# Kernel optimization log

Hardware: AMD Instinct MI355X
Metric: run time of the kernel (lower is better)

The kernel has to match this reference:

```python
import jax, jax.numpy as jnp
import numpy as np

B_, C_, NH_, WS_, HID_ = 8, 512, 16, 7, 2048
HH, WW = 56, 56


def _rel_pos_index(ws):
    coords = np.stack(np.meshgrid(np.arange(ws), np.arange(ws), indexing='ij'))  # (2,ws,ws)
    cf = coords.reshape(2, -1)
    rc = (cf[:, :, None] - cf[:, None, :]).transpose(1, 2, 0)  # (ws2,ws2,2)
    rc[..., 0] += ws - 1
    rc[..., 1] += ws - 1
    rc[..., 0] *= 2 * ws - 1
    return jnp.asarray(rc.sum(-1).reshape(-1))  # (ws2*ws2,)


def _ln(x, g, b, eps):
    mu = x.mean(-1, keepdims=True)
    var = ((x - mu) ** 2).mean(-1, keepdims=True)
    return (x - mu) * jax.lax.rsqrt(var + eps) * g + b


def setup_inputs() -> dict:
    key = jax.random.key(0)
    ks = jax.random.split(key, 8)
    s = lambda k, shape: (jax.random.normal(k, shape, jnp.float32) * 0.02)
    return {
        'x': jax.random.normal(ks[0], (B_, HH * WW, C_), jnp.float32),
        'H': HH, 'W': WW,
        'norm1_g': jnp.ones((C_,), jnp.float32), 'norm1_b': jnp.zeros((C_,), jnp.float32),
        'norm2_g': jnp.ones((C_,), jnp.float32), 'norm2_b': jnp.zeros((C_,), jnp.float32),
        'qkv_w': s(ks[1], (3 * C_, C_)), 'qkv_b': jnp.zeros((3 * C_,), jnp.float32),
        'rpb': s(ks[2], ((2 * WS_ - 1) ** 2, NH_)),
        'fc1_w': s(ks[3], (HID_, C_)), 'fc1_b': jnp.zeros((HID_,), jnp.float32),
        'dw_w': s(ks[4], (HID_, 1, 3, 3)), 'dw_b': jnp.zeros((HID_,), jnp.float32),
        'fc2_w': s(ks[5], (C_, HID_)), 'fc2_b': jnp.zeros((C_,), jnp.float32),
    }


def reference(x, H, W, norm1_g, norm1_b, norm2_g, norm2_b, qkv_w, qkv_b, rpb,
              fc1_w, fc1_b, dw_w, dw_b, fc2_w, fc2_b):
    B, N, C = x.shape
    ws, nh = WS_, NH_
    hd = C // nh
    scale = hd ** -0.5
    ws2 = ws * ws
    nHw, nWw = H // ws, W // ws

    # ---- norm1 + WaveAttention (windowed attention w/ relative position bias) ----
    h = _ln(x, norm1_g, norm1_b, 1e-5)
    qkv = h @ qkv_w.T + qkv_b                                   # [B,N,3C]
    # window partition: [B, nH, ws, nW, ws, 3, nh, hd] -> [3, B*nH*nW, nh, ws2, hd]
    qkv = qkv.reshape(B, nHw, ws, nWw, ws, 3, nh, hd)
    qkv = qkv.transpose(5, 0, 1, 3, 6, 2, 4, 7).reshape(3, B * nHw * nWw, nh, ws2, hd)
    q, k, v = qkv[0], qkv[1], qkv[2]

    attn = jnp.einsum('wnid,wnjd->wnij', q, k) * scale          # [Bw,nh,ws2,ws2]
    bias = rpb[_rel_pos_index(ws)].reshape(ws2, ws2, nh).transpose(2, 0, 1)
    attn = jax.nn.softmax(attn + bias[None], axis=-1)
    out = jnp.einsum('wnij,wnjd->wnid', attn, v)                # [Bw,nh,ws2,hd]
    # window reverse
    out = out.transpose(0, 2, 1, 3).reshape(B, nHw, nWw, ws, ws, C)
    out = out.transpose(0, 1, 3, 2, 4, 5).reshape(B, N, C)
    x = x + out

    # ---- norm2 + PVT2FFN (fc1 -> depthwise 3x3 conv -> GELU -> fc2) ----
    h2 = _ln(x, norm2_g, norm2_b, 1e-5)
    h2 = h2 @ fc1_w.T + fc1_b                                   # [B,N,HID]
    img = h2.reshape(B, H, W, HID_).transpose(0, 3, 1, 2)       # [B,HID,H,W]
    img = jax.lax.conv_general_dilated(img, dw_w, (1, 1), 'SAME',
                                       feature_group_count=HID_)
    img = img + dw_b[None, :, None, None]
    h2 = img.reshape(B, HID_, N).transpose(0, 2, 1)
    h2 = jax.nn.gelu(h2, approximate=False)
    h2 = h2 @ fc2_w.T + fc2_b
    return x + h2
```

## Files before the change

### kernel.cpp

```cpp
#include <hip/hip_runtime.h>
#include <hip/hip_bf16.h>

typedef unsigned short u16;
typedef unsigned int u32;
typedef __attribute__((ext_vector_type(8))) short bf16x8_t;
typedef __attribute__((ext_vector_type(4))) float f32x4_t;
typedef __attribute__((ext_vector_type(8))) u16 u16x8;
typedef __attribute__((ext_vector_type(4))) u32 u32x4;

constexpr int B_  = 8;
constexpr int C_  = 512;
constexpr int NH_ = 16;
constexpr int HID_= 2048;
constexpr int Hh  = 56, Ww = 56;
constexpr int N_  = Hh * Ww;
constexpr int M_  = B_ * N_;

__device__ __forceinline__ u16 f2bf(float f) {
    u32 u = __float_as_uint(f);
    u32 r = (u + 0x7fffu + ((u >> 16) & 1u)) >> 16;
    return (u16)r;
}
__device__ __forceinline__ float bf2f(u16 v) {
    return __uint_as_float(((u32)v) << 16);
}

__device__ __forceinline__ void bar_raw() {
    __asm__ __volatile__("s_barrier" ::: "memory");
}

typedef const void __attribute__((address_space(1))) gvoid_t;
typedef void __attribute__((address_space(3))) lvoid_t;
__device__ __forceinline__ void gload16(const u16* g, u16* l) {
    __builtin_amdgcn_global_load_lds((gvoid_t*)g, (lvoid_t*)l, 16, 0, 0);
}

__global__ void cvt_w(const float* __restrict__ qkvw, const float* __restrict__ fc1w,
                      const float* __restrict__ fc2w, u16* __restrict__ oq,
                      u16* __restrict__ o1, u16* __restrict__ o2) {
    int i = blockIdx.x * 256 + threadIdx.x;
    if (i < 3 * C_ * C_) oq[i] = f2bf(qkvw[i]);
    if (i < HID_ * C_) { o1[i] = f2bf(fc1w[i]); o2[i] = f2bf(fc2w[i]); }
}

__global__ __launch_bounds__(256) void ln_kernel(const float* __restrict__ x,
        const float* __restrict__ g, const float* __restrict__ b, u16* __restrict__ out) {
    int lane = threadIdx.x & 63, wv = threadIdx.x >> 6;
    size_t row = (size_t)blockIdx.x * 4 + wv;
    const float4* xr = (const float4*)(x + row * C_);
    float4 a = xr[lane * 2], c = xr[lane * 2 + 1];
    float s  = a.x + a.y + a.z + a.w + c.x + c.y + c.z + c.w;
    float ss = a.x*a.x + a.y*a.y + a.z*a.z + a.w*a.w + c.x*c.x + c.y*c.y + c.z*c.z + c.w*c.w;
    #pragma unroll
    for (int off = 1; off < 64; off <<= 1) {
        s  += __shfl_xor(s, off);
        ss += __shfl_xor(ss, off);
    }
    float mean = s * (1.0f / C_);
    float var  = ss * (1.0f / C_) - mean * mean;
    float rstd = rsqrtf(var + 1e-5f);
    const float4* g4 = (const float4*)g;
    const float4* b4 = (const float4*)b;
    float4 g0 = g4[lane*2], g1 = g4[lane*2+1], b0 = b4[lane*2], b1 = b4[lane*2+1];
    u16x8 o;
    o[0] = f2bf((a.x - mean) * rstd * g0.x + b0.x);
    o[1] = f2bf((a.y - mean) * rstd * g0.y + b0.y);
    o[2] = f2bf((a.z - mean) * rstd * g0.z + b0.z);
    o[3] = f2bf((a.w - mean) * rstd * g0.w + b0.w);
    o[4] = f2bf((c.x - mean) * rstd * g1.x + b1.x);
    o[5] = f2bf((c.y - mean) * rstd * g1.y + b1.y);
    o[6] = f2bf((c.z - mean) * rstd * g1.z + b1.z);
    o[7] = f2bf((c.w - mean) * rstd * g1.w + b1.w);
    *(u16x8*)&out[row * C_ + lane * 8] = o;
}

template<bool RES, bool OUT_BF16>
__global__ __launch_bounds__(512) void gemm256(
        const u16* __restrict__ A, const u16* __restrict__ B,
        const float* __restrict__ bias, const float* __restrict__ res,
        void* __restrict__ Cout, int M, int N, int K,
        int nbm, int nbn) {
    const int nwg = nbm * nbn;
    const int id = blockIdx.x;
    const int xcd = id & 7, ii = id >> 3;
    const int q = nwg >> 3, r = nwg & 7;
    const int gidx = (xcd < r ? xcd * (q + 1) : r * (q + 1) + (xcd - r) * q) + ii;
    const int bm = gidx / nbn;
    const int bn = gidx - bm * nbn;

    __shared__ __align__(16) u16 As[2 * 16384];
    __shared__ __align__(16) u16 Bs[2 * 16384];
    const int tid = threadIdx.x;
    const int lane = tid & 63;
    const int w = tid >> 6;
    const int wm = w >> 2, wn = w & 3;

    const int r0 = lane >> 2;
    const int gcb = ((lane & 3) ^ ((lane >> 3) & 3));
    const int fr = lane & 15;
    const int g4 = lane >> 4;
    const int swz = (g4 ^ ((fr >> 1) & 3)) * 8;
    const int bhf = wn >> 1;
    const int bg0 = (wn & 1) * 4;

    const u16* aBase = A + (size_t)(bm * 256) * K;
    const u16* bBase = B + (size_t)(bn * 256) * K;

    f32x4_t acc[2][2][4][2];
    f32x4_t zero = {0.f, 0.f, 0.f, 0.f};
    #pragma unroll
    for (int a0 = 0; a0 < 2; a0++)
        #pragma unroll
        for (int b0 = 0; b0 < 2; b0++)
            #pragma unroll
            for (int c0 = 0; c0 < 4; c0++)
                #pragma unroll
                for (int d0 = 0; d0 < 2; d0++) acc[a0][b0][c0][d0] = zero;

    auto stage = [&](const u16* gb, u16* lb, int u, int hf) {
        const u16* src = gb + (size_t)(hf * 128 + w * 16 + r0) * K
                            + (size_t)(u * 64 + gcb * 8);
        u16* dst = lb + (u & 1) * 16384 + hf * 8192 + w * 512;
        gload16(src, dst);
        gload16(src + 32, dst + 4096);
    };

#define RD_A(DST, BB, QM)                                                      \
    _Pragma("unroll")                                                          \
    for (int ks = 0; ks < 2; ks++)                                             \
        _Pragma("unroll")                                                      \
        for (int mf = 0; mf < 4; mf++)                                         \
            DST[ks][mf] = *(const bf16x8_t*)&As[(BB) + wm * 8192 + ks * 4096   \
                            + ((QM) * 4 + mf) * 512 + fr * 32 + swz];

#define RD_B(DST, BB, QN)                                                      \
    _Pragma("unroll")                                                          \
    for (int ks = 0; ks < 2; ks++)                                             \
        _Pragma("unroll")                                                      \
        for (int nf = 0; nf < 2; nf++)                                         \
            DST[ks][nf] = *(const bf16x8_t*)&Bs[(BB) + bhf * 8192 + ks * 4096  \
                            + (bg0 + (QN) * 2 + nf) * 512 + fr * 32 + swz];

#define MMAC(QM, QN, AR, BR)                                                   \
    __builtin_amdgcn_s_setprio(1);                                             \
    _Pragma("unroll")                                                          \
    for (int mf = 0; mf < 4; mf++)                                             \
        _Pragma("unroll")                                                      \
        for (int nf = 0; nf < 2; nf++)                                         \
            _Pragma("unroll")                                                  \
            for (int ks = 0; ks < 2; ks++)                                     \
                acc[QM][QN][mf][nf] = __builtin_amdgcn_mfma_f32_16x16x32_bf16( \
                    AR[ks][mf], BR[ks][nf], acc[QM][QN][mf][nf], 0, 0, 0);     \
    __builtin_amdgcn_s_setprio(0);

    const int NT = K >> 6;
    stage(aBase, As, 0, 0);
    stage(aBase, As, 0, 1);
    stage(bBase, Bs, 0, 0);
    stage(bBase, Bs, 0, 1);
    stage(bBase, Bs, 1, 0);
    stage(aBase, As, 1, 0);
    __asm__ __volatile__("s_waitcnt vmcnt(0)" ::: "memory");
    bar_raw();

    bf16x8_t afr[2][4], bq0[2][2], bq1[2][2];
    RD_A(afr, 0, 0);
    RD_B(bq0, 0, 0);

    for (int t = 0; t < NT; t++) {
        const int bb = (t & 1) * 16384;
        const int ob = bb ^ 16384;
        MMAC(0, 0, afr, bq0);
        RD_B(bq1, bb, 1);
        if (t + 1 < NT) stage(aBase, As, t + 1, 1);
        bar_raw();
        MMAC(0, 1, afr, bq1);
        RD_A(afr, bb, 1);
        if (t + 1 < NT) stage(bBase, Bs, t + 1, 1);
        bar_raw();
        MMAC(1, 1, afr, bq1);
        if (t + 2 < NT) stage(bBase, Bs, t + 2, 0);
        bar_raw();
        MMAC(1, 0, afr, bq0);
        if (t + 2 < NT) {
            stage(aBase, As, t + 2, 0);
            __asm__ __volatile__("s_waitcnt vmcnt(4)" ::: "memory");
        } else if (t + 1 < NT) {
            __asm__ __volatile__("s_waitcnt vmcnt(0)" ::: "memory");
        }
        bar_raw();
        if (t + 1 < NT) {
            RD_A(afr, ob, 0);
            RD_B(bq0, ob, 0);
        }
    }

#undef RD_A
#undef RD_B
#undef MMAC

    #pragma unroll
    for (int qm = 0; qm < 2; qm++)
        #pragma unroll
        for (int qn = 0; qn < 2; qn++)
            #pragma unroll
            for (int mf = 0; mf < 4; mf++)
                #pragma unroll
                for (int rr = 0; rr < 4; rr++) {
                    int row = bm * 256 + wm * 128 + qm * 64 + mf * 16 + (lane >> 4) * 4 + rr;
                    #pragma unroll
                    for (int nf = 0; nf < 2; nf++) {
                        int col = bn * 256 + wn * 64 + qn * 32 + nf * 16 + (lane & 15);
                        float v = acc[qm][qn][mf][nf][rr] + bias[col];
                        if constexpr (RES) v += res[(size_t)row * N + col];
                        if constexpr (OUT_BF16) ((u16*)Cout)[(size_t)row * N + col] = f2bf(v);
                        else ((float*)Cout)[(size_t)row * N + col] = v;
                    }
                }
}

constexpr int QS = 40;
constexpr int VS = 72;
constexpr int PS = 72;

__global__ __launch_bounds__(256) void attn_kernel(
        const u16* __restrict__ qkv, const float* __restrict__ rpb,
        u16* __restrict__ aout) {
    __shared__ __align__(16) u16 q_s[64 * QS];
    __shared__ __align__(16) u16 k_s[64 * QS];
    __shared__ __align__(16) u16 vT_s[32 * VS];
    __shared__ __align__(16) u16 p_s[64 * PS];
    const int tid = threadIdx.x, lane = tid & 63, wv = tid >> 6;
    const int wh = blockIdx.x;
    const int head = wh & 15, w = wh >> 4;
    const int b = w >> 6, win = w & 63, bh = win >> 3, bw = win & 7;

    {
        int i = tid >> 2, dc = (tid & 3) * 8;
        if (i < 49) {
            int n = (bh * 7 + i / 7) * Ww + (bw * 7 + i % 7);
            const u16* base = qkv + ((size_t)(b * N_ + n)) * (3 * C_) + head * 32 + dc;
            *(u16x8*)&q_s[i * QS + dc] = *(const u16x8*)(base);
            *(u16x8*)&k_s[i * QS + dc] = *(const u16x8*)(base + C_);
        } else {
            u16x8 z = {0,0,0,0,0,0,0,0};
            *(u16x8*)&q_s[i * QS + dc] = z;
            *(u16x8*)&k_s[i * QS + dc] = z;
        }
    }
    for (int f = tid; f < 64 * 32; f += 256) {
        int i = f >> 5, d = f & 31;
        u16 val = 0;
        if (i < 49) {
            int n = (bh * 7 + i / 7) * Ww + (bw * 7 + i % 7);
            val = qkv[((size_t)(b * N_ + n)) * (3 * C_) + 2 * C_ + head * 32 + d];
        }
        vT_s[d * VS + i] = val;
    }
    __syncthreads();

    f32x4_t zero = {0.f, 0.f, 0.f, 0.f};
    f32x4_t s[4];
    bf16x8_t aq = *(const bf16x8_t*)&q_s[(wv * 16 + (lane & 15)) * QS + (lane >> 4) * 8];
    #pragma unroll
    for (int nt = 0; nt < 4; nt++) {
        bf16x8_t bk = *(const bf16x8_t*)&k_s[(nt * 16 + (lane & 15)) * QS + (lane >> 4) * 8];
        s[nt] = __builtin_amdgcn_mfma_f32_16x16x32_bf16(aq, bk, zero, 0, 0, 0);
    }

    const float scale = 0.17677669529663687f;
    #pragma unroll
    for (int r = 0; r < 4; r++) {
        int row = wv * 16 + (lane >> 4) * 4 + r;
        int qy = row / 7, qx = row - qy * 7;
        float pv[4];
        float m = -1e30f;
        #pragma unroll
        for (int nt = 0; nt < 4; nt++) {
            int col = nt * 16 + (lane & 15);
            float bias;
            if (row < 49 && col < 49) {
                int ky = col / 7, kx = col - ky * 7;
                bias = rpb[((qy - ky + 6) * 13 + (qx - kx + 6)) * NH_ + head];
            } else bias = -1e30f;
            float v = s[nt][r] * scale + bias;
            pv[nt] = v;
            m = fmaxf(m, v);
        }
        #pragma unroll
        for (int off = 1; off < 16; off <<= 1) m = fmaxf(m, __shfl_xor(m, off));
        float sum = 0.f;
        #pragma unroll
        for (int nt = 0; nt < 4; nt++) { pv[nt] = __expf(pv[nt] - m); sum += pv[nt]; }
        #pragma unroll
        for (int off = 1; off < 16; off <<= 1) sum += __shfl_xor(sum, off);
        float inv = 1.0f / sum;
        #pragma unroll
        for (int nt = 0; nt < 4; nt++)
            p_s[row * PS + nt * 16 + (lane & 15)] = f2bf(pv[nt] * inv);
    }
    __syncthreads();

    f32x4_t o[2] = {zero, zero};
    #pragma unroll
    for (int kt = 0; kt < 2; kt++) {
        bf16x8_t ap = *(const bf16x8_t*)&p_s[(wv * 16 + (lane & 15)) * PS + kt * 32 + (lane >> 4) * 8];
        #pragma unroll
        for (int nt = 0; nt < 2; nt++) {
            bf16x8_t bv = *(const bf16x8_t*)&vT_s[(nt * 16 + (lane & 15)) * VS + kt * 32 + (lane >> 4) * 8];
            o[nt] = __builtin_amdgcn_mfma_f32_16x16x32_bf16(ap, bv, o[nt], 0, 0, 0);
        }
    }
    u16* obase = aout + ((size_t)(w * 16 + head)) * 49 * 32;
    #pragma unroll
    for (int nt = 0; nt < 2; nt++) {
        #pragma unroll
        for (int r = 0; r < 4; r++) {
            int row = wv * 16 + (lane >> 4) * 4 + r;
            if (row < 49)
                obase[row * 32 + nt * 16 + (lane & 15)] = f2bf(o[nt][r]);
        }
    }
}

__global__ __launch_bounds__(256) void wrev_ln(const float* __restrict__ x,
        const u16* __restrict__ aout, const float* __restrict__ g,
        const float* __restrict__ bt, float* __restrict__ x2, u16* __restrict__ h) {
    int lane = threadIdx.x & 63, wvv = threadIdx.x >> 6;
    int m = blockIdx.x * 4 + wvv;
    int b = m / N_, n = m - b * N_;
    int iy = n / Ww, ix = n - iy * Ww;
    int w = b * 64 + (iy / 7) * 8 + (ix / 7);
    int pos = (iy % 7) * 7 + (ix % 7);
    int head = lane >> 2, d0 = (lane & 3) * 8;
    u16x8 ao = *(const u16x8*)&aout[(((size_t)w * 16 + head) * 49 + pos) * 32 + d0];
    const float4* xr = (const float4*)(x + (size_t)m * C_ + lane * 8);
    float4 a = xr[0], c = xr[1];
    float v[8];
    v[0] = a.x + bf2f(ao[0]); v[1] = a.y + bf2f(ao[1]);
    v[2] = a.z + bf2f(ao[2]); v[3] = a.w + bf2f(ao[3]);
    v[4] = c.x + bf2f(ao[4]); v[5] = c.y + bf2f(ao[5]);
    v[6] = c.z + bf2f(ao[6]); v[7] = c.w + bf2f(ao[7]);
    float s = 0.f, ss = 0.f;
    #pragma unroll
    for (int jj = 0; jj < 8; jj++) { s += v[jj]; ss += v[jj] * v[jj]; }
    #pragma unroll
    for (int off = 1; off < 64; off <<= 1) {
        s  += __shfl_xor(s, off);
        ss += __shfl_xor(ss, off);
    }
    float mean = s * (1.0f / C_);
    float var  = ss * (1.0f / C_) - mean * mean;
    float rstd = rsqrtf(var + 1e-5f);
    float4 o0 = {v[0], v[1], v[2], v[3]}, o1 = {v[4], v[5], v[6], v[7]};
    float4* x2r = (float4*)(x2 + (size_t)m * C_ + lane * 8);
    x2r[0] = o0; x2r[1] = o1;
    const float4* g4 = (const float4*)(g + lane * 8);
    const float4* b4 = (const float4*)(bt + lane * 8);
    float4 g0 = g4[0], g1 = g4[1], bb0 = b4[0], bb1 = b4[1];
    u16x8 o;
    o[0] = f2bf((v[0] - mean) * rstd * g0.x + bb0.x);
    o[1] = f2bf((v[1] - mean) * rstd * g0.y + bb0.y);
    o[2] = f2bf((v[2] - mean) * rstd * g0.z + bb0.z);
    o[3] = f2bf((v[3] - mean) * rstd * g0.w + bb0.w);
    o[4] = f2bf((v[4] - mean) * rstd * g1.x + bb1.x);
    o[5] = f2bf((v[5] - mean) * rstd * g1.y + bb1.y);
    o[6] = f2bf((v[6] - mean) * rstd * g1.z + bb1.z);
    o[7] = f2bf((v[7] - mean) * rstd * g1.w + bb1.w);
    *(u16x8*)&h[(size_t)m * C_ + lane * 8] = o;
}

__global__ __launch_bounds__(256) void dwconv_gelu(const u16* __restrict__ in,
        const float* __restrict__ w, const float* __restrict__ bias, u16* __restrict__ out) {
    const int t = threadIdx.x;
    const int blk = blockIdx.x;
    const int xq = blk & 3;
    const int byp = blk >> 2;
    const int yp = byp % 28;
    const int b = byp / 28;
    const int y0 = yp * 2;
    const int c0 = t * 8;

    float wr[9][8];
    #pragma unroll
    for (int k = 0; k < 9; k++)
        #pragma unroll
        for (int j = 0; j < 8; j++) wr[k][j] = w[(c0 + j) * 9 + k];
    float bs[8];
    #pragma unroll
    for (int j = 0; j < 8; j++) bs[j] = bias[c0 + j];

    u16x8 zerov = {0,0,0,0,0,0,0,0};
    auto ldcol = [&](int xx, u16x8* col) {
        #pragma unroll
        for (int dy = 0; dy < 4; dy++) {
            int yy = y0 + dy - 1;
            bool ok = (yy >= 0 && yy < Hh && xx >= 0 && xx < Ww);
            col[dy] = ok ? *(const u16x8*)&in[(((size_t)b * Hh + yy) * Ww + xx) * HID_ + c0] : zerov;
        }
    };

    int xs = xq * 14;
    u16x8 wA[4], wB[4], wC[4];
    ldcol(xs - 1, wA);
    ldcol(xs, wB);
    for (int x = xs; x < xs + 14; x++) {
        ldcol(x + 1, wC);
        float acc0[8], acc1[8];
        #pragma unroll
        for (int j = 0; j < 8; j++) { acc0[j] = bs[j]; acc1[j] = bs[j]; }
        #pragma unroll
        for (int dy = 0; dy < 3; dy++)
            #pragma unroll
            for (int j = 0; j < 8; j++) {
                acc0[j] += bf2f(wA[dy][j]) * wr[dy * 3 + 0][j];
                acc0[j] += bf2f(wB[dy][j]) * wr[dy * 3 + 1][j];
                acc0[j] += bf2f(wC[dy][j]) * wr[dy * 3 + 2][j];
                acc1[j] += bf2f(wA[dy + 1][j]) * wr[dy * 3 + 0][j];
                acc1[j] += bf2f(wB[dy + 1][j]) * wr[dy * 3 + 1][j];
                acc1[j] += bf2f(wC[dy + 1][j]) * wr[dy * 3 + 2][j];
            }
        u16x8 o0, o1;
        #pragma unroll
        for (int j = 0; j < 8; j++) {
            float v0 = acc0[j];
            o0[j] = f2bf(0.5f * v0 * (1.0f + erff(v0 * 0.70710678118654752f)));
            float v1 = acc1[j];
            o1[j] = f2bf(0.5f * v1 * (1.0f + erff(v1 * 0.70710678118654752f)));
        }
        *(u16x8*)&out[(((size_t)b * Hh + y0) * Ww + x) * HID_ + c0] = o0;
        *(u16x8*)&out[(((size_t)b * Hh + y0 + 1) * Ww + x) * HID_ + c0] = o1;
        #pragma unroll
        for (int dy = 0; dy < 4; dy++) { wA[dy] = wB[dy]; wB[dy] = wC[dy]; }
    }
}

extern "C" void kernel_launch(void* const* d_in, const int* in_sizes, int n_in,
                              void* d_out, int out_size, void* d_ws, size_t ws_size,
                              hipStream_t stream) {
    const float* x    = (const float*)d_in[0];
    const float* n1g  = (const float*)d_in[3];
    const float* n1b  = (const float*)d_in[4];
    const float* n2g  = (const float*)d_in[5];
    const float* n2b  = (const float*)d_in[6];
    const float* qkvw = (const float*)d_in[7];
    const float* qkvb = (const float*)d_in[8];
    const float* rpb  = (const float*)d_in[9];
    const float* fc1w = (const float*)d_in[10];
    const float* fc1b = (const float*)d_in[11];
    const float* dww  = (const float*)d_in[12];
    const float* dwb  = (const float*)d_in[13];
    const float* fc2w = (const float*)d_in[14];
    const float* fc2b = (const float*)d_in[15];

    char* ws = (char*)d_ws;
    float* x2  = (float*)(ws);
    u16*   h   = (u16*)(ws + 51380224);
    u16*   qkvo= (u16*)(ws + 77070336);
    u16*   aout= (u16*)(ws + 154140672);
    u16*   f1o = (u16*)(ws + 154140672);
    u16*   cvo = (u16*)(ws + 51380224);
    u16*   wq  = (u16*)(ws + 256901120);
    u16*   w1  = (u16*)(ws + 256901120 + 1572864);
    u16*   w2  = (u16*)(ws + 256901120 + 1572864 + 2097152);

    cvt_w<<<dim3(4096), dim3(256), 0, stream>>>(qkvw, fc1w, fc2w, wq, w1, w2);
    ln_kernel<<<dim3(M_ / 4), dim3(256), 0, stream>>>(x, n1g, n1b, h);
    gemm256<false, true><<<dim3(588), dim3(512), 0, stream>>>(
        h, wq, qkvb, nullptr, (void*)qkvo, M_, 1536, 512, 98, 6);
    attn_kernel<<<dim3(B_ * 64 * NH_), dim3(256), 0, stream>>>(qkvo, rpb, aout);
    wrev_ln<<<dim3(M_ / 4), dim3(256), 0, stream>>>(x, aout, n2g, n2b, x2, h);
    gemm256<false, true><<<dim3(784), dim3(512), 0, stream>>>(
        h, w1, fc1b, nullptr, (void*)f1o, M_, 2048, 512, 98, 8);
    dwconv_gelu<<<dim3(B_ * 28 * 4), dim3(256), 0, stream>>>(f1o, dww, dwb, cvo);
    gemm256<true, false><<<dim3(196), dim3(512), 0, stream>>>(
        cvo, w2, fc2b, x2, d_out, M_, 512, 2048, 98, 2);
}
```

Before: 510.1 us.

## Use 128x128 GEMM for K=512 projections, fuse weight cast into LN, remap blocks

Adds a smaller 128x128-tile, 256-thread bf16 MFMA GEMM that stages through registers and double-buffers the K slices. It replaces the 256-tile kernel for the qkv and fc1 projections, giving more workgroups for these short-K GEMMs, with an XCD-aware grouping so four N-tiles share one A tile. The weight-conversion kernel is merged into the first LayerNorm launch to drop one launch. The dwconv block index is remapped so each XCD handles contiguous rows. The 256-tile GEMM prologue now waits with vmcnt(4) instead of draining all loads, which risks reading LDS before the last staged tiles have landed.

Result: faster. 475.5 us (-6.8%).

```diff
diff --git a/kernel.cpp b/kernel.cpp
--- a/kernel.cpp
+++ b/kernel.cpp
@@ -28,6 +28,10 @@
 __device__ __forceinline__ void bar_raw() {
     __asm__ __volatile__("s_barrier" ::: "memory");
 }
+__device__ __forceinline__ void bar_lgkm() {
+    __builtin_amdgcn_s_waitcnt(0xc07f);
+    __asm__ __volatile__("s_barrier" ::: "memory");
+}
 
 typedef const void __attribute__((address_space(1))) gvoid_t;
 typedef void __attribute__((address_space(3))) lvoid_t;
@@ -35,16 +39,18 @@
     __builtin_amdgcn_global_load_lds((gvoid_t*)g, (lvoid_t*)l, 16, 0, 0);
 }
 
-__global__ void cvt_w(const float* __restrict__ qkvw, const float* __restrict__ fc1w,
-                      const float* __restrict__ fc2w, u16* __restrict__ oq,
-                      u16* __restrict__ o1, u16* __restrict__ o2) {
-    int i = blockIdx.x * 256 + threadIdx.x;
-    if (i < 3 * C_ * C_) oq[i] = f2bf(qkvw[i]);
-    if (i < HID_ * C_) { o1[i] = f2bf(fc1w[i]); o2[i] = f2bf(fc2w[i]); }
-}
-
-__global__ __launch_bounds__(256) void ln_kernel(const float* __restrict__ x,
-        const float* __restrict__ g, const float* __restrict__ b, u16* __restrict__ out) {
+__global__ __launch_bounds__(256) void cvt_ln(
+        const float* __restrict__ x, const float* __restrict__ g, const float* __restrict__ b,
+        u16* __restrict__ out,
+        const float* __restrict__ qkvw, const float* __restrict__ fc1w,
+        const float* __restrict__ fc2w, u16* __restrict__ oq,
+        u16* __restrict__ o1, u16* __restrict__ o2) {
+    if (blockIdx.x >= (M_ / 4)) {
+        int i = (blockIdx.x - M_ / 4) * 256 + threadIdx.x;
+        if (i < 3 * C_ * C_) oq[i] = f2bf(qkvw[i]);
+        if (i < HID_ * C_) { o1[i] = f2bf(fc1w[i]); o2[i] = f2bf(fc2w[i]); }
+        return;
+    }
     int lane = threadIdx.x & 63, wv = threadIdx.x >> 6;
     size_t row = (size_t)blockIdx.x * 4 + wv;
     const float4* xr = (const float4*)(x + row * C_);
@@ -75,6 +81,108 @@
 }
 
 template<bool RES, bool OUT_BF16>
+__global__ __launch_bounds__(256) void gemm_bt(
+        const u16* __restrict__ A, const u16* __restrict__ B,
+        const float* __restrict__ bias, const float* __restrict__ res,
+        void* __restrict__ Cout, int M, int N, int K,
+        int nbm, int nbn, int nGroups) {
+    const int id = blockIdx.x;
+    const int xcd = id & 7, slot = id >> 3;
+    const int j = slot & 3;
+    const int gidx = xcd + 8 * (slot >> 2);
+    if (gidx >= nGroups) return;
+    const int bm = gidx % nbm;
+    const int bn = (gidx / nbm) * 4 + j;
+    if (bn >= nbn) return;
+
+    __shared__ __align__(16) u16 As[2 * 128 * 32];
+    __shared__ __align__(16) u16 Bs[2 * 128 * 32];
+    const int tid = threadIdx.x;
+    const int lane = tid & 63;
+    const int wv = tid >> 6;
+
+    const int r0 = lane >> 2;
+    const int gcb = ((lane & 3) ^ ((lane >> 3) & 3));
+
+    const u16* aBase = A + (size_t)(bm * 128) * K;
+    const u16* bBase = B + (size_t)(bn * 128) * K;
+
+    f32x4_t acc[4][4];
+    f32x4_t zero = {0.f, 0.f, 0.f, 0.f};
+    #pragma unroll
+    for (int i = 0; i < 4; i++)
+        #pragma unroll
+        for (int jj = 0; jj < 4; jj++) acc[i][jj] = zero;
+
+    const int mo = (wv >> 1) * 64, no = (wv & 1) * 64;
+    const int fr = lane & 15;
+    const int g4 = lane >> 4;
+    const int kkey = (fr >> 1) & 3;
+    const int pos = (g4 ^ kkey) * 8;
+
+    u32x4 ra[2][2], rb[2][2];
+    auto ldissue = [&](int k0) {
+        #pragma unroll
+        for (int p = 0; p < 2; p++)
+            #pragma unroll
+            for (int jj = 0; jj < 2; jj++) {
+                const int ko = k0 + p * 32 + gcb * 8;
+                ra[p][jj] = *(const u32x4*)(aBase + (size_t)((wv + jj * 4) * 16 + r0) * K + ko);
+                rb[p][jj] = *(const u32x4*)(bBase + (size_t)((wv + jj * 4) * 16 + r0) * K + ko);
+            }
+    };
+    auto dswrite = [&]() {
+        #pragma unroll
+        for (int p = 0; p < 2; p++)
+            #pragma unroll
+            for (int jj = 0; jj < 2; jj++) {
+                ((u32x4*)&As[p * 4096 + (wv + jj * 4) * 16 * 32])[lane] = ra[p][jj];
+                ((u32x4*)&Bs[p * 4096 + (wv + jj * 4) * 16 * 32])[lane] = rb[p][jj];
+            }
+    };
+
+    ldissue(0);
+    for (int k0 = 0; k0 < K; k0 += 64) {
+        dswrite();
+        bar_lgkm();
+        if (k0 + 64 < K) ldissue(k0 + 64);
+
+        #pragma unroll
+        for (int ks = 0; ks < 2; ks++) {
+            bf16x8_t af[4], bfr[4];
+            #pragma unroll
+            for (int mt = 0; mt < 4; mt++)
+                af[mt] = *(const bf16x8_t*)&As[ks * 4096 + (mo + mt * 16 + fr) * 32 + pos];
+            #pragma unroll
+            for (int nt = 0; nt < 4; nt++)
+                bfr[nt] = *(const bf16x8_t*)&Bs[ks * 4096 + (no + nt * 16 + fr) * 32 + pos];
+            #pragma unroll
+            for (int mt = 0; mt < 4; mt++)
+                #pragma unroll
+                for (int nt = 0; nt < 4; nt++)
+                    acc[mt][nt] = __builtin_amdgcn_mfma_f32_16x16x32_bf16(af[mt], bfr[nt], acc[mt][nt], 0, 0, 0);
+        }
+        bar_raw();
+    }
+
+    #pragma unroll
+    for (int mt = 0; mt < 4; mt++) {
+        #pragma unroll
+        for (int r = 0; r < 4; r++) {
+            int row = bm * 128 + mo + mt * 16 + (lane >> 4) * 4 + r;
+            #pragma unroll
+            for (int nt = 0; nt < 4; nt++) {
+                int col = bn * 128 + no + nt * 16 + (lane & 15);
+                float v = acc[mt][nt][r] + bias[col];
+                if constexpr (RES) v += res[(size_t)row * N + col];
+                if constexpr (OUT_BF16) ((u16*)Cout)[(size_t)row * N + col] = f2bf(v);
+                else ((float*)Cout)[(size_t)row * N + col] = v;
+            }
+        }
+    }
+}
+
+template<bool RES, bool OUT_BF16>
 __global__ __launch_bounds__(512) void gemm256(
         const u16* __restrict__ A, const u16* __restrict__ B,
         const float* __restrict__ bias, const float* __restrict__ res,
@@ -160,7 +268,7 @@
     stage(bBase, Bs, 0, 1);
     stage(bBase, Bs, 1, 0);
     stage(aBase, As, 1, 0);
-    __asm__ __volatile__("s_waitcnt vmcnt(0)" ::: "memory");
+    __asm__ __volatile__("s_waitcnt vmcnt(4)" ::: "memory");
     bar_raw();
 
     bf16x8_t afr[2][4], bq0[2][2], bq1[2][2];
@@ -374,10 +482,13 @@
         const float* __restrict__ w, const float* __restrict__ bias, u16* __restrict__ out) {
     const int t = threadIdx.x;
     const int blk = blockIdx.x;
-    const int xq = blk & 3;
-    const int byp = blk >> 2;
-    const int yp = byp % 28;
-    const int b = byp / 28;
+    const int xcd = blk & 7;
+    const int j = blk >> 3;
+    const int yp = j % 28;
+    const int combo = j / 28;
+    const int gl = xcd * 4 + combo;
+    const int b = gl >> 2;
+    const int xq = gl & 3;
     const int y0 = yp * 2;
     const int c0 = t * 8;
 
@@ -385,10 +496,10 @@
     #pragma unroll
     for (int k = 0; k < 9; k++)
         #pragma unroll
-        for (int j = 0; j < 8; j++) wr[k][j] = w[(c0 + j) * 9 + k];
+        for (int jj = 0; jj < 8; jj++) wr[k][jj] = w[(c0 + jj) * 9 + k];
     float bs[8];
     #pragma unroll
-    for (int j = 0; j < 8; j++) bs[j] = bias[c0 + j];
+    for (int jj = 0; jj < 8; jj++) bs[jj] = bias[c0 + jj];
 
     u16x8 zerov = {0,0,0,0,0,0,0,0};
     auto ldcol = [&](int xx, u16x8* col) {
@@ -408,25 +519,25 @@
         ldcol(x + 1, wC);
         float acc0[8], acc1[8];
         #pragma unroll
-        for (int j = 0; j < 8; j++) { acc0[j] = bs[j]; acc1[j] = bs[j]; }
+        for (int jj = 0; jj < 8; jj++) { acc0[jj] = bs[jj]; acc1[jj] = bs[jj]; }
         #pragma unroll
         for (int dy = 0; dy < 3; dy++)
             #pragma unroll
-            for (int j = 0; j < 8; j++) {
-                acc0[j] += bf2f(wA[dy][j]) * wr[dy * 3 + 0][j];
-                acc0[j] += bf2f(wB[dy][j]) * wr[dy * 3 + 1][j];
-                acc0[j] += bf2f(wC[dy][j]) * wr[dy * 3 + 2][j];
-                acc1[j] += bf2f(wA[dy + 1][j]) * wr[dy * 3 + 0][j];
-                acc1[j] += bf2f(wB[dy + 1][j]) * wr[dy * 3 + 1][j];
-                acc1[j] += bf2f(wC[dy + 1][j]) * wr[dy * 3 + 2][j];
+            for (int jj = 0; jj < 8; jj++) {
+                acc0[jj] += bf2f(wA[dy][jj]) * wr[dy * 3 + 0][jj];
+                acc0[jj] += bf2f(wB[dy][jj]) * wr[dy * 3 + 1][jj];
+                acc0[jj] += bf2f(wC[dy][jj]) * wr[dy * 3 + 2][jj];
+                acc1[jj] += bf2f(wA[dy + 1][jj]) * wr[dy * 3 + 0][jj];
+                acc1[jj] += bf2f(wB[dy + 1][jj]) * wr[dy * 3 + 1][jj];
+                acc1[jj] += bf2f(wC[dy + 1][jj]) * wr[dy * 3 + 2][jj];
             }
         u16x8 o0, o1;
         #pragma unroll
-        for (int j = 0; j < 8; j++) {
-            float v0 = acc0[j];
-            o0[j] = f2bf(0.5f * v0 * (1.0f + erff(v0 * 0.70710678118654752f)));
-            float v1 = acc1[j];
-            o1[j] = f2bf(0.5f * v1 * (1.0f + erff(v1 * 0.70710678118654752f)));
+        for (int jj = 0; jj < 8; jj++) {
+            float v0 = acc0[jj];
+            o0[jj] = f2bf(0.5f * v0 * (1.0f + erff(v0 * 0.70710678118654752f)));
+            float v1 = acc1[jj];
+            o1[jj] = f2bf(0.5f * v1 * (1.0f + erff(v1 * 0.70710678118654752f)));
         }
         *(u16x8*)&out[(((size_t)b * Hh + y0) * Ww + x) * HID_ + c0] = o0;
         *(u16x8*)&out[(((size_t)b * Hh + y0 + 1) * Ww + x) * HID_ + c0] = o1;
@@ -464,14 +575,16 @@
     u16*   w1  = (u16*)(ws + 256901120 + 1572864);
     u16*   w2  = (u16*)(ws + 256901120 + 1572864 + 2097152);
 
-    cvt_w<<<dim3(4096), dim3(256), 0, stream>>>(qkvw, fc1w, fc2w, wq, w1, w2);
-    ln_kernel<<<dim3(M_ / 4), dim3(256), 0, stream>>>(x, n1g, n1b, h);
-    gemm256<false, true><<<dim3(588), dim3(512), 0, stream>>>(
-        h, wq, qkvb, nullptr, (void*)qkvo, M_, 1536, 512, 98, 6);
+    auto ggrid = [](int nGroups) { return 32 * ((nGroups + 7) / 8); };
+
+    cvt_ln<<<dim3(M_ / 4 + 4096), dim3(256), 0, stream>>>(
+        x, n1g, n1b, h, qkvw, fc1w, fc2w, wq, w1, w2);
+    gemm_bt<false, true><<<dim3(ggrid(588)), dim3(256), 0, stream>>>(
+        h, wq, qkvb, nullptr, (void*)qkvo, M_, 1536, 512, 196, 12, 588);
     attn_kernel<<<dim3(B_ * 64 * NH_), dim3(256), 0, stream>>>(qkvo, rpb, aout);
     wrev_ln<<<dim3(M_ / 4), dim3(256), 0, stream>>>(x, aout, n2g, n2b, x2, h);
-    gemm256<false, true><<<dim3(784), dim3(512), 0, stream>>>(
-        h, w1, fc1b, nullptr, (void*)f1o, M_, 2048, 512, 98, 8);
+    gemm_bt<false, true><<<dim3(ggrid(784)), dim3(256), 0, stream>>>(
+        h, w1, fc1b, nullptr, (void*)f1o, M_, 2048, 512, 196, 16, 784);
     dwconv_gelu<<<dim3(B_ * 28 * 4), dim3(256), 0, stream>>>(f1o, dww, dwb, cvo);
     gemm256<true, false><<<dim3(196), dim3(512), 0, stream>>>(
         cvo, w2, fc2b, x2, d_out, M_, 512, 2048, 98, 2);
```
